# Performance work log

Measured on AMD Instinct MI355X. Metric: run time of the kernel, lower is better.

The kernel has to match this reference:

```python
import jax, jax.numpy as jnp
import numpy as np


def setup_inputs() -> dict:
    key = jax.random.key(0)
    ks = jax.random.split(key, 5)
    B, T, S, D = 4, 32, 320, 768
    return {
        "x": jax.random.normal(ks[0], (B, T, S, D), dtype=jnp.float32),
        "qkv_w": jax.random.normal(ks[1], (D, 3 * D), dtype=jnp.float32) * 0.02,
        "qkv_b": jax.random.normal(ks[2], (3 * D,), dtype=jnp.float32) * 0.02,
        "out_w": jax.random.normal(ks[3], (D, D), dtype=jnp.float32) * 0.02,
        "out_b": jax.random.normal(ks[4], (D,), dtype=jnp.float32) * 0.02,
        "n_latents": 64,
        "n_heads": 12,
    }


def reference(x, qkv_w, qkv_b, out_w, out_b, n_latents, n_heads):
    B, T, S, D = x.shape
    H = n_heads
    hd = D // H
    scale = 1.0 / jnp.sqrt(jnp.asarray(hd, dtype=x.dtype))

    # qkv projection: [B,T,S,3D]
    qkv = jnp.einsum('btsd,de->btse', x, qkv_w) + qkv_b
    q, k, v = jnp.split(qkv, 3, axis=-1)
    # [B,T,S,H,hd]
    q = q.reshape(B, T, S, H, hd)
    k = k.reshape(B, T, S, H, hd)
    v = v.reshape(B, T, S, H, hd)

    # block-sparse mask: latent queries (rows < n_latents) cannot attend to
    # patch keys (cols >= n_latents); everything else allowed
    rows = jnp.arange(S) < n_latents          # latent query rows
    cols = jnp.arange(S) >= n_latents         # patch key cols
    allow = ~(rows[:, None] & cols[None, :])  # [S,S] bool

    # attention scores [B,T,H,Sq,Sk]
    scores = jnp.einsum('btqhd,btkhd->bthqk', q, k) * scale
    scores = jnp.where(allow, scores, -jnp.inf)
    attn = jax.nn.softmax(scores, axis=-1)

    y = jnp.einsum('bthqk,btkhd->btqhd', attn, v).reshape(B, T, S, D)
    return jnp.einsum('btsd,de->btse', y, out_w) + out_b
```

## Files before the change

### kernel.cpp

```cpp
#include <hip/hip_runtime.h>

typedef __attribute__((ext_vector_type(8))) short bf16x8;
typedef __attribute__((ext_vector_type(4))) float f32x4;
typedef __attribute__((ext_vector_type(16))) float f32x16;
typedef __attribute__((address_space(1))) void gvoid_t;
typedef __attribute__((address_space(3))) void lvoid_t;

#define DEVI __device__ __forceinline__
#define SB __builtin_amdgcn_sched_barrier(0)

DEVI unsigned short f2bf(float f) {
    unsigned int u = __builtin_bit_cast(unsigned int, f);
    u += 0x7fffu + ((u >> 16) & 1u);
    return (unsigned short)(u >> 16);
}

DEVI unsigned cvt_pk_bf16(float a, float b) {
    unsigned r;
    asm("v_cvt_pk_bf16_f32 %0, %1, %2" : "=v"(r) : "v"(a), "v"(b));
    return r;
}

DEVI f32x4 mfma16(bf16x8 a, bf16x8 b, f32x4 c) {
    return __builtin_amdgcn_mfma_f32_16x16x32_bf16(a, b, c, 0, 0, 0);
}

__global__ void k_convert(const float* __restrict__ in, unsigned short* __restrict__ out, int n8) {
    int i = blockIdx.x * 256 + threadIdx.x;
    if (i >= n8) return;
    const float4* p = (const float4*)in + (size_t)i * 2;
    float4 a = p[0], b = p[1];
    uint4 o;
    o.x = f2bf(a.x) | ((unsigned)f2bf(a.y) << 16);
    o.y = f2bf(a.z) | ((unsigned)f2bf(a.w) << 16);
    o.z = f2bf(b.x) | ((unsigned)f2bf(b.y) << 16);
    o.w = f2bf(b.z) | ((unsigned)f2bf(b.w) << 16);
    *((uint4*)out + i) = o;
}

__global__ void k_transpose(const float* __restrict__ w, unsigned short* __restrict__ wt, int K, int N) {
    __shared__ float tile[32][33];
    int n0 = blockIdx.x * 32, k0 = blockIdx.y * 32;
    int tx = threadIdx.x, ty = threadIdx.y;
#pragma unroll
    for (int r = 0; r < 32; r += 8)
        tile[ty + r][tx] = w[(size_t)(k0 + ty + r) * N + n0 + tx];
    __syncthreads();
#pragma unroll
    for (int r = 0; r < 32; r += 8)
        wt[(size_t)(n0 + ty + r) * K + k0 + tx] = f2bf(tile[tx][ty + r]);
}

__global__ __launch_bounds__(256) void k_kpack(const unsigned short* __restrict__ qkv,
                                               unsigned short* __restrict__ kp) {
    int bht = blockIdx.x;
    int t = bht % 10, bh = bht / 10;
    int h = bh % 12, bt = bh / 12;
    int c = threadIdx.x >> 6, l = threadIdx.x & 63;
    const unsigned short* src = qkv + (size_t)(bt * 320 + t * 32 + (l & 31)) * 2304
                                + 768 + h * 64 + c * 16 + (l >> 5) * 8;
    uint4 v = *(const uint4*)src;
    *(uint4*)(kp + ((size_t)bht * 4 + c) * 512 + l * 8) = v;
}

template <bool OUT_BF16>
__global__ __launch_bounds__(512, 2) void k_gemm256(const unsigned short* __restrict__ A,
                                                    const unsigned short* __restrict__ Bt,
                                                    const float* __restrict__ bias,
                                                    void* __restrict__ out,
                                                    int M, int N, int K) {
    __shared__ unsigned short smem[65536];

    const int tid = threadIdx.x;
    const int nwg = gridDim.x, bid = blockIdx.x;
    const int q8 = nwg >> 3, r8 = nwg & 7;
    const int xcd = bid & 7, lid = bid >> 3;
    const int swz = ((xcd < r8) ? xcd * (q8 + 1) : r8 * (q8 + 1) + (xcd - r8) * q8) + lid;
    const int ntn = N >> 8;
    const int bm = swz / ntn, bn = swz % ntn;

    const int lane = tid & 63, wid = tid >> 6;
    const int wr = wid >> 2, wc = wid & 3;
    const int lr = lane & 15, lg = lane >> 4;
    const int cswz = (lr & 7) << 3;
    const int col0 = (lg * 8) ^ cswz;

    const int NT = K >> 6;

    const int srowl = tid >> 3;
    const int scole = ((tid & 7) ^ (srowl & 7)) << 3;
    const unsigned short* aSrc = A  + (size_t)(bm * 256 + srowl) * K + scole;
    const unsigned short* bSrc = Bt + (size_t)(bn * 256 + srowl) * K + scole;

#define STG(matOff, srcBase, qq, koff, bufw)                                              \
    __builtin_amdgcn_global_load_lds((gvoid_t*)((srcBase) + (size_t)(qq) * 64 * K + (koff)), \
        (lvoid_t*)(smem + (matOff) + (bufw) * 16384 + (qq) * 4096 + tid * 8), 16, 0, 0)
#define LDA(mf, base, rowoff, kk) \
    *(const bf16x8*)((base) + ((rowoff) + (mf) * 16 + lr) * 64 + (col0 ^ ((kk) * 32)))

    f32x4 acc[8][4];
#pragma unroll
    for (int i = 0; i < 8; ++i)
#pragma unroll
        for (int j = 0; j < 4; ++j) acc[i][j] = (f32x4){0.f, 0.f, 0.f, 0.f};

    {
        const int k1 = (NT > 1) ? 64 : 0;
        STG(0, aSrc, 0, 0, 0); STG(0, aSrc, 1, 0, 0); STG(0, aSrc, 2, 0, 0); STG(0, aSrc, 3, 0, 0);
        STG(32768, bSrc, 0, 0, 0); STG(32768, bSrc, 1, 0, 0); STG(32768, bSrc, 2, 0, 0); STG(32768, bSrc, 3, 0, 0);
        STG(0, aSrc, 0, k1, 1); STG(0, aSrc, 2, k1, 1);
        asm volatile("s_waitcnt vmcnt(2)" ::: "memory");
        __builtin_amdgcn_s_barrier();
    }

#pragma unroll 1
    for (int t = 0; t < NT; ++t) {
        const int bufR = t & 1, bufW = bufR ^ 1;
        const int ko1 = (t + 1 < NT) ? (t + 1) * 64 : 0;
        const int ko2 = (t + 2 < NT) ? (t + 2) * 64 : 0;
        const unsigned short* abuf = smem + bufR * 16384;
        const unsigned short* bbuf = smem + 32768 + bufR * 16384;
        bf16x8 afv[4][2], b01[2][2], b23[2][2];

#pragma unroll
        for (int j = 0; j < 2; ++j)
#pragma unroll
            for (int kk = 0; kk < 2; ++kk)
                b01[j][kk] = LDA(j, bbuf, wc * 64, kk);
#pragma unroll
        for (int mf = 0; mf < 2; ++mf)
#pragma unroll
            for (int kk = 0; kk < 2; ++kk)
                afv[mf][kk] = LDA(mf, abuf, wr * 128, kk);
        SB;
#pragma unroll
        for (int mf = 2; mf < 4; ++mf)
#pragma unroll
            for (int kk = 0; kk < 2; ++kk)
                afv[mf][kk] = LDA(mf, abuf, wr * 128, kk);
        SB;
        STG(32768, bSrc, 0, ko1, bufW); STG(32768, bSrc, 1, ko1, bufW);
        asm volatile("s_waitcnt lgkmcnt(4)" ::: "memory"); SB;
        __builtin_amdgcn_s_setprio(1);
#pragma unroll
        for (int mf = 0; mf < 2; ++mf)
#pragma unroll
            for (int j = 0; j < 2; ++j)
#pragma unroll
                for (int kk = 0; kk < 2; ++kk)
                    acc[mf][j] = mfma16(afv[mf][kk], b01[j][kk], acc[mf][j]);
        __builtin_amdgcn_s_setprio(0);
        asm volatile("s_waitcnt lgkmcnt(0)" ::: "memory"); SB;
        __builtin_amdgcn_s_setprio(1);
#pragma unroll
        for (int mf = 2; mf < 4; ++mf)
#pragma unroll
            for (int j = 0; j < 2; ++j)
#pragma unroll
                for (int kk = 0; kk < 2; ++kk)
                    acc[mf][j] = mfma16(afv[mf][kk], b01[j][kk], acc[mf][j]);
        __builtin_amdgcn_s_setprio(0);

#pragma unroll
        for (int kk = 0; kk < 2; ++kk)
            b23[0][kk] = LDA(2, bbuf, wc * 64, kk);
        SB;
#pragma unroll
        for (int kk = 0; kk < 2; ++kk)
            b23[1][kk] = LDA(3, bbuf, wc * 64, kk);
        SB;
        STG(32768, bSrc, 2, ko1, bufW); STG(32768, bSrc, 3, ko1, bufW);
        asm volatile("s_waitcnt lgkmcnt(2)" ::: "memory"); SB;
        __builtin_amdgcn_s_setprio(1);
#pragma unroll
        for (int mf = 0; mf < 4; ++mf)
#pragma unroll
            for (int kk = 0; kk < 2; ++kk)
                acc[mf][2] = mfma16(afv[mf][kk], b23[0][kk], acc[mf][2]);
        __builtin_amdgcn_s_setprio(0);
        asm volatile("s_waitcnt lgkmcnt(0)" ::: "memory"); SB;
        __builtin_amdgcn_s_setprio(1);
#pragma unroll
        for (int mf = 0; mf < 4; ++mf)
#pragma unroll
            for (int kk = 0; kk < 2; ++kk)
                acc[mf][3] = mfma16(afv[mf][kk], b23[1][kk], acc[mf][3]);
        __builtin_amdgcn_s_setprio(0);

#pragma unroll
        for (int mf = 0; mf < 2; ++mf)
#pragma unroll
            for (int kk = 0; kk < 2; ++kk)
                afv[mf][kk] = LDA(mf, abuf, wr * 128 + 64, kk);
        SB;
#pragma unroll
        for (int mf = 2; mf < 4; ++mf)
#pragma unroll
            for (int kk = 0; kk < 2; ++kk)
                afv[mf][kk] = LDA(mf, abuf, wr * 128 + 64, kk);
        SB;
        STG(0, aSrc, 1, ko1, bufW); STG(0, aSrc, 3, ko1, bufW);
        asm volatile("s_waitcnt lgkmcnt(4)" ::: "memory"); SB;
        __builtin_amdgcn_s_setprio(1);
#pragma unroll
        for (int mf = 0; mf < 2; ++mf)
#pragma unroll
            for (int j = 0; j < 2; ++j)
#pragma unroll
                for (int kk = 0; kk < 2; ++kk)
                    acc[4 + mf][2 + j] = mfma16(afv[mf][kk], b23[j][kk], acc[4 + mf][2 + j]);
        __builtin_amdgcn_s_setprio(0);
        asm volatile("s_waitcnt lgkmcnt(0)" ::: "memory"); SB;
        __builtin_amdgcn_s_setprio(1);
#pragma unroll
        for (int mf = 2; mf < 4; ++mf)
#pragma unroll
            for (int j = 0; j < 2; ++j)
#pragma unroll
                for (int kk = 0; kk < 2; ++kk)
                    acc[4 + mf][2 + j] = mfma16(afv[mf][kk], b23[j][kk], acc[4 + mf][2 + j]);
        __builtin_amdgcn_s_setprio(0);

        __builtin_amdgcn_s_setprio(1);
#pragma unroll
        for (int mf = 0; mf < 4; ++mf)
#pragma unroll
            for (int j = 0; j < 2; ++j)
#pragma unroll
                for (int kk = 0; kk < 2; ++kk)
                    acc[4 + mf][j] = mfma16(afv[mf][kk], b01[j][kk], acc[4 + mf][j]);
        __builtin_amdgcn_s_setprio(0);
        asm volatile("s_waitcnt vmcnt(0)" ::: "memory");
        __builtin_amdgcn_s_barrier();
        STG(0, aSrc, 0, ko2, bufR); STG(0, aSrc, 2, ko2, bufR);
    }
#undef STG
#undef LDA

    asm volatile("s_waitcnt vmcnt(0)" ::: "memory");
    __syncthreads();
    float bv[4];
#pragma unroll
    for (int nf = 0; nf < 4; ++nf)
        bv[nf] = bias[bn * 256 + wc * 64 + nf * 16 + lr];

    if (OUT_BF16) {
        unsigned short* ebuf = smem + wid * 8192;
#pragma unroll
        for (int h = 0; h < 2; ++h) {
#pragma unroll
            for (int mf4 = 0; mf4 < 4; ++mf4) {
                int mf = h * 4 + mf4;
#pragma unroll
                for (int nf = 0; nf < 4; ++nf)
#pragma unroll
                    for (int i = 0; i < 4; ++i)
                        ebuf[(mf4 * 16 + lg * 4 + i) * 72 + nf * 16 + lr] = f2bf(acc[mf][nf][i] + bv[nf]);
            }
            asm volatile("s_waitcnt lgkmcnt(0)" ::: "memory"); SB;
#pragma unroll
            for (int ps = 0; ps < 8; ++ps) {
                int rl = ps * 8 + (lane >> 3), ck = lane & 7;
                uint4 vv = *(const uint4*)&ebuf[rl * 72 + ck * 8];
                int grow = bm * 256 + wr * 128 + h * 64 + rl;
                int gcol = bn * 256 + wc * 64 + ck * 8;
                *(uint4*)&((unsigned short*)out)[(size_t)grow * N + gcol] = vv;
            }
            asm volatile("s_waitcnt lgkmcnt(0)" ::: "memory"); SB;
        }
    } else {
        float* ebuf = (float*)smem + wid * 4096;
#pragma unroll
        for (int qq = 0; qq < 4; ++qq) {
#pragma unroll
            for (int m2 = 0; m2 < 2; ++m2) {
                int mf = qq * 2 + m2;
#pragma unroll
                for (int nf = 0; nf < 4; ++nf)
#pragma unroll
                    for (int i = 0; i < 4; ++i)
                        ebuf[(m2 * 16 + lg * 4 + i) * 68 + nf * 16 + lr] = acc[mf][nf][i] + bv[nf];
            }
            asm volatile("s_waitcnt lgkmcnt(0)" ::: "memory"); SB;
#pragma unroll
            for (int ps = 0; ps < 8; ++ps) {
                int rl = ps * 4 + (lane >> 4), ck = lane & 15;
                uint4 vv = *(const uint4*)&ebuf[rl * 68 + ck * 4];
                int grow = bm * 256 + wr * 128 + qq * 32 + rl;
                int gcol = bn * 256 + wc * 64 + ck * 4;
                *(uint4*)&((float*)out)[(size_t)grow * N + gcol] = vv;
            }
            asm volatile("s_waitcnt lgkmcnt(0)" ::: "memory"); SB;
        }
    }
}

__global__ __launch_bounds__(640) void k_attn5(const unsigned short* __restrict__ qkv,
                                               const unsigned short* __restrict__ kp,
                                               unsigned short* __restrict__ y) {
    int bt = blockIdx.x / 12, h = blockIdx.x % 12;
    const unsigned short* Qg = qkv + (size_t)bt * 320 * 2304 + h * 64;
    const unsigned short* Vg = Qg + 1536;
    const unsigned short* Kpb = kp + (size_t)blockIdx.x * 20480;

    __shared__ unsigned short Vt[10 * 64 * 40];

    int tid = threadIdx.x, w = tid >> 6, l = tid & 63;
    int q = l & 31, hh = l >> 5;
    int q0 = w * 32;
    int ntile = (w < 2) ? 2 : 10;

    {
        int k = tid >> 1;
        int tt = k >> 5, sk = k & 31;
        int d0 = (tid & 1) * 32;
        const unsigned short* src = Vg + (size_t)k * 2304 + d0;
#pragma unroll
        for (int c = 0; c < 4; ++c) {
            union { uint4 u; unsigned short s[8]; } vv;
            vv.u = *(const uint4*)(src + c * 8);
#pragma unroll
            for (int j = 0; j < 8; ++j) {
                int d = d0 + c * 8 + j;
                Vt[(tt * 64 + d) * 40 + (sk ^ (((d >> 3) & 3) << 3))] = vv.s[j];
            }
        }
    }

    bf16x8 qf[4];
#pragma unroll
    for (int c = 0; c < 4; ++c)
        qf[c] = *(const bf16x8*)(Qg + (size_t)(q0 + q) * 2304 + c * 16 + hh * 8);

    f32x16 o0 = (f32x16)0.f, o1 = (f32x16)0.f;
    float m = -3e38f, lsum = 0.f;
    const float SC = 0.125f * 1.44269504089f;

    bf16x8 kfA[4], kfB[4];
    auto loadK = [&](bf16x8 (&kf)[4], int tt) {
#pragma unroll
        for (int c = 0; c < 4; ++c)
            kf[c] = *(const bf16x8*)(Kpb + tt * 2048 + c * 512 + l * 8);
    };
    loadK(kfA, 0);

    __syncthreads();

    auto process = [&](int t, bf16x8 (&kf)[4]) {
        f32x16 sacc = (f32x16)0.f;
#pragma unroll
        for (int c = 0; c < 4; ++c)
            sacc = __builtin_amdgcn_mfma_f32_32x32x16_bf16(kf[c], qf[c], sacc, 0, 0, 0);

        float p[16];
#pragma unroll
        for (int r = 0; r < 16; ++r) p[r] = sacc[r] * SC;
        float tm = fmaxf(
            fmaxf(fmaxf(fmaxf(p[0], p[1]), fmaxf(p[2], p[3])),
                  fmaxf(fmaxf(p[4], p[5]), fmaxf(p[6], p[7]))),
            fmaxf(fmaxf(fmaxf(p[8], p[9]), fmaxf(p[10], p[11])),
                  fmaxf(fmaxf(p[12], p[13]), fmaxf(p[14], p[15]))));
        tm = fmaxf(tm, __shfl_xor(tm, 32));
        if (!__all(tm <= m + 8.f)) {
            float mn = fmaxf(m, tm);
            float al = __builtin_amdgcn_exp2f(m - mn);
            lsum *= al;
#pragma unroll
            for (int r = 0; r < 16; ++r) { o0[r] *= al; o1[r] *= al; }
            m = mn;
        }
#pragma unroll
        for (int r = 0; r < 16; ++r) p[r] = __builtin_amdgcn_exp2f(p[r] - m);
        float rs =
            ((p[0] + p[1]) + (p[2] + p[3])) + ((p[4] + p[5]) + (p[6] + p[7])) +
            (((p[8] + p[9]) + (p[10] + p[11])) + ((p[12] + p[13]) + (p[14] + p[15])));
        lsum += rs;

        unsigned a0 = cvt_pk_bf16(p[0], p[1]);
        unsigned a1 = cvt_pk_bf16(p[2], p[3]);
        unsigned b0 = cvt_pk_bf16(p[4], p[5]);
        unsigned b1 = cvt_pk_bf16(p[6], p[7]);
        asm("v_permlane32_swap_b32 %0, %1" : "+v"(a0), "+v"(b0));
        asm("v_permlane32_swap_b32 %0, %1" : "+v"(a1), "+v"(b1));
        unsigned c0 = cvt_pk_bf16(p[8], p[9]);
        unsigned c1 = cvt_pk_bf16(p[10], p[11]);
        unsigned d0 = cvt_pk_bf16(p[12], p[13]);
        unsigned d1 = cvt_pk_bf16(p[14], p[15]);
        asm("v_permlane32_swap_b32 %0, %1" : "+v"(c0), "+v"(d0));
        asm("v_permlane32_swap_b32 %0, %1" : "+v"(c1), "+v"(d1));
        union { unsigned u[4]; bf16x8 v; } pf0, pf1;
        pf0.u[0] = a0; pf0.u[1] = a1; pf0.u[2] = b0; pf0.u[3] = b1;
        pf1.u[0] = c0; pf1.u[1] = c1; pf1.u[2] = d0; pf1.u[3] = d1;

        const unsigned short* vt = Vt + t * 2560;
        {
            int d = q;
            int sw = (d >> 3) & 3;
            bf16x8 va0 = *(const bf16x8*)&vt[d * 40 + ((0 + hh) ^ sw) * 8];
            bf16x8 va1 = *(const bf16x8*)&vt[d * 40 + ((2 + hh) ^ sw) * 8];
            o0 = __builtin_amdgcn_mfma_f32_32x32x16_bf16(va0, pf0.v, o0, 0, 0, 0);
            o0 = __builtin_amdgcn_mfma_f32_32x32x16_bf16(va1, pf1.v, o0, 0, 0, 0);
        }
        {
            int d = 32 + q;
            int sw = (d >> 3) & 3;
            bf16x8 va0 = *(const bf16x8*)&vt[d * 40 + ((0 + hh) ^ sw) * 8];
            bf16x8 va1 = *(const bf16x8*)&vt[d * 40 + ((2 + hh) ^ sw) * 8];
            o1 = __builtin_amdgcn_mfma_f32_32x32x16_bf16(va0, pf0.v, o1, 0, 0, 0);
            o1 = __builtin_amdgcn_mfma_f32_32x32x16_bf16(va1, pf1.v, o1, 0, 0, 0);
        }
    };

    for (int t = 0; t < ntile; t += 2) {
        loadK(kfB, t + 1);
        process(t, kfA);
        loadK(kfA, (t + 2 < 10) ? (t + 2) : 8);
        process(t + 1, kfB);
    }

    lsum += __shfl_xor(lsum, 32);
    float inv = 1.f / lsum;
    unsigned short* yp = y + (size_t)(bt * 320 + q0 + q) * 768 + h * 64;
#pragma unroll
    for (int r = 0; r < 16; r += 2) {
        int dr = (r & 3) + 8 * (r >> 2) + 4 * hh;
        *(unsigned*)(yp + dr) =
            (unsigned)f2bf(o0[r] * inv) | ((unsigned)f2bf(o0[r + 1] * inv) << 16);
        *(unsigned*)(yp + 32 + dr) =
            (unsigned)f2bf(o1[r] * inv) | ((unsigned)f2bf(o1[r + 1] * inv) << 16);
    }
}

extern "C" void kernel_launch(void* const* d_in, const int* in_sizes, int n_in,
                              void* d_out, int out_size, void* d_ws, size_t ws_size,
                              hipStream_t stream) {
    const float* x     = (const float*)d_in[0];
    const float* qkv_w = (const float*)d_in[1];
    const float* qkv_b = (const float*)d_in[2];
    const float* out_w = (const float*)d_in[3];
    const float* out_b = (const float*)d_in[4];

    const int M = 40960;
    unsigned short* xb  = (unsigned short*)d_ws;
    unsigned short* w1t = xb + (size_t)M * 768;
    unsigned short* w2t = w1t + (size_t)2304 * 768;
    unsigned short* qkv = w2t + (size_t)768 * 768;
    unsigned short* yb  = qkv + (size_t)M * 2304;
    unsigned short* kp  = xb;

    k_convert<<<(M * 768 / 8 + 255) / 256, 256, 0, stream>>>(x, xb, M * 768 / 8);
    k_transpose<<<dim3(2304 / 32, 768 / 32), dim3(32, 8), 0, stream>>>(qkv_w, w1t, 768, 2304);
    k_transpose<<<dim3(768 / 32, 768 / 32), dim3(32, 8), 0, stream>>>(out_w, w2t, 768, 768);

    k_gemm256<true><<<(M / 256) * (2304 / 256), 512, 0, stream>>>(xb, w1t, qkv_b, (void*)qkv, M, 2304, 768);
    k_kpack<<<1536 * 10, 256, 0, stream>>>(qkv, kp);
    k_attn5<<<128 * 12, 640, 0, stream>>>(qkv, kp, yb);
    k_gemm256<false><<<(M / 256) * (768 / 256), 512, 0, stream>>>(yb, w2t, out_b, d_out, M, 768, 768);
}
```

Baseline: 378.3 us.

## Rework GEMM global-load issue order and attention V-transpose and K loading

In the GEMM main loop, all global-to-LDS stage loads for the next k-step are now issued at once early in the iteration instead of spread across sub-phases, aiming to get memory traffic in flight sooner. The attention kernel gets launch bounds with a minimum-occupancy hint. Its V transpose now reads 4x4 sub-blocks and writes packed 32-bit pairs to LDS instead of scalar 16-bit stores. The double-buffered K register prefetch is replaced by a simple per-tile load. These changes reduce LDS store count and register pressure, at the risk of exposing K load latency and of the GEMM's lgkmcnt wait counts no longer matching the number of outstanding operations.

Measured after the change: 384.0 us. Within noise of the previous version (+1.5%).

```diff
diff --git a/kernel.cpp b/kernel.cpp
--- a/kernel.cpp
+++ b/kernel.cpp
@@ -140,6 +140,8 @@
                 afv[mf][kk] = LDA(mf, abuf, wr * 128, kk);
         SB;
         STG(32768, bSrc, 0, ko1, bufW); STG(32768, bSrc, 1, ko1, bufW);
+        STG(32768, bSrc, 2, ko1, bufW); STG(32768, bSrc, 3, ko1, bufW);
+        STG(0, aSrc, 1, ko1, bufW); STG(0, aSrc, 3, ko1, bufW);
         asm volatile("s_waitcnt lgkmcnt(4)" ::: "memory"); SB;
         __builtin_amdgcn_s_setprio(1);
 #pragma unroll
@@ -169,7 +171,6 @@
         for (int kk = 0; kk < 2; ++kk)
             b23[1][kk] = LDA(3, bbuf, wc * 64, kk);
         SB;
-        STG(32768, bSrc, 2, ko1, bufW); STG(32768, bSrc, 3, ko1, bufW);
         asm volatile("s_waitcnt lgkmcnt(2)" ::: "memory"); SB;
         __builtin_amdgcn_s_setprio(1);
 #pragma unroll
@@ -199,7 +200,6 @@
             for (int kk = 0; kk < 2; ++kk)
                 afv[mf][kk] = LDA(mf, abuf, wr * 128 + 64, kk);
         SB;
-        STG(0, aSrc, 1, ko1, bufW); STG(0, aSrc, 3, ko1, bufW);
         asm volatile("s_waitcnt lgkmcnt(4)" ::: "memory"); SB;
         __builtin_amdgcn_s_setprio(1);
 #pragma unroll
@@ -295,9 +295,9 @@
     }
 }
 
-__global__ __launch_bounds__(640) void k_attn5(const unsigned short* __restrict__ qkv,
-                                               const unsigned short* __restrict__ kp,
-                                               unsigned short* __restrict__ y) {
+__global__ __launch_bounds__(640, 5) void k_attn6(const unsigned short* __restrict__ qkv,
+                                                  const unsigned short* __restrict__ kp,
+                                                  unsigned short* __restrict__ y) {
     int bt = blockIdx.x / 12, h = blockIdx.x % 12;
     const unsigned short* Qg = qkv + (size_t)bt * 320 * 2304 + h * 64;
     const unsigned short* Vg = Qg + 1536;
@@ -310,20 +310,26 @@
     int q0 = w * 32;
     int ntile = (w < 2) ? 2 : 10;
 
-    {
-        int k = tid >> 1;
-        int tt = k >> 5, sk = k & 31;
-        int d0 = (tid & 1) * 32;
-        const unsigned short* src = Vg + (size_t)k * 2304 + d0;
-#pragma unroll
-        for (int c = 0; c < 4; ++c) {
-            union { uint4 u; unsigned short s[8]; } vv;
-            vv.u = *(const uint4*)(src + c * 8);
-#pragma unroll
-            for (int j = 0; j < 8; ++j) {
-                int d = d0 + c * 8 + j;
-                Vt[(tt * 64 + d) * 40 + (sk ^ (((d >> 3) & 3) << 3))] = vv.s[j];
-            }
+#pragma unroll
+    for (int it = 0; it < 2; ++it) {
+        int blk = tid + it * 640;
+        int tt = blk >> 7, rr = blk & 127;
+        int k0 = (rr & 7) * 4;
+        int d0 = (rr >> 3) * 4;
+        const unsigned short* src = Vg + (size_t)(tt * 32 + k0) * 2304 + d0;
+        union { uint2 u; unsigned short s[4]; } r0, r1, r2, r3;
+        r0.u = *(const uint2*)(src);
+        r1.u = *(const uint2*)(src + 2304);
+        r2.u = *(const uint2*)(src + 4608);
+        r3.u = *(const uint2*)(src + 6912);
+#pragma unroll
+        for (int dd = 0; dd < 4; ++dd) {
+            int d = d0 + dd;
+            int sw = ((d >> 3) & 3) << 3;
+            uint2 o;
+            o.x = (unsigned)r0.s[dd] | ((unsigned)r1.s[dd] << 16);
+            o.y = (unsigned)r2.s[dd] | ((unsigned)r3.s[dd] << 16);
+            *(uint2*)&Vt[(size_t)(tt * 64 + d) * 40 + (k0 ^ sw)] = o;
         }
     }
 
@@ -336,17 +342,14 @@
     float m = -3e38f, lsum = 0.f;
     const float SC = 0.125f * 1.44269504089f;
 
-    bf16x8 kfA[4], kfB[4];
-    auto loadK = [&](bf16x8 (&kf)[4], int tt) {
+    __syncthreads();
+
+    for (int t = 0; t < ntile; ++t) {
+        bf16x8 kf[4];
 #pragma unroll
         for (int c = 0; c < 4; ++c)
-            kf[c] = *(const bf16x8*)(Kpb + tt * 2048 + c * 512 + l * 8);
-    };
-    loadK(kfA, 0);
-
-    __syncthreads();
-
-    auto process = [&](int t, bf16x8 (&kf)[4]) {
+            kf[c] = *(const bf16x8*)(Kpb + t * 2048 + c * 512 + l * 8);
+
         f32x16 sacc = (f32x16)0.f;
 #pragma unroll
         for (int c = 0; c < 4; ++c)
@@ -409,13 +412,6 @@
             o1 = __builtin_amdgcn_mfma_f32_32x32x16_bf16(va0, pf0.v, o1, 0, 0, 0);
             o1 = __builtin_amdgcn_mfma_f32_32x32x16_bf16(va1, pf1.v, o1, 0, 0, 0);
         }
-    };
-
-    for (int t = 0; t < ntile; t += 2) {
-        loadK(kfB, t + 1);
-        process(t, kfA);
-        loadK(kfA, (t + 2 < 10) ? (t + 2) : 8);
-        process(t + 1, kfB);
     }
 
     lsum += __shfl_xor(lsum, 32);
@@ -454,6 +450,6 @@
 
     k_gemm256<true><<<(M / 256) * (2304 / 256), 512, 0, stream>>>(xb, w1t, qkv_b, (void*)qkv, M, 2304, 768);
     k_kpack<<<1536 * 10, 256, 0, stream>>>(qkv, kp);
-    k_attn5<<<128 * 12, 640, 0, stream>>>(qkv, kp, yb);
+    k_attn6<<<128 * 12, 640, 0, stream>>>(qkv, kp, yb);
     k_gemm256<false><<<(M / 256) * (768 / 256), 512, 0, stream>>>(yb, w2t, out_b, d_out, M, 768, 768);
 }
```
